# Optimization experiments

Measured on AMD Instinct MI355X. Metric: run time of the kernel, lower is better.

Reference implementation:

```python
import jax, jax.numpy as jnp
import numpy as np
from functools import partial

BLUR_K = 5
SIGMA = 1.5
DOWN = 4
SCALE = 5.0
OFFSET = 0.2

_DN = ('NCHW', 'OIHW', 'NCHW')


def _gaussian_kernel(k, sigma):
    x = jnp.arange(k, dtype=jnp.float32) - (k - 1) / 2.0
    g = jnp.exp(-x ** 2 / (2.0 * sigma ** 2))
    g2 = jnp.outer(g, g)
    g2 = g2 / g2.sum()
    return g2.reshape(1, 1, k, k)


def setup_inputs() -> dict:
    key = jax.random.key(0)
    left_rgb = jax.random.uniform(key, (16, 3, 544, 960), dtype=jnp.float32)
    return {"left_rgb": left_rgb}


def reference(left_rgb):
    B, C, H, W = left_rgb.shape
    # rgb -> gray (1x1 conv with fixed weights)
    w = jnp.array([0.2989, 0.587, 0.114], dtype=left_rgb.dtype)
    gray = jnp.einsum('bchw,c->bhw', left_rgb, w)[:, None]  # [B,1,H,W]

    # gaussian blur with reflect padding (torch F.pad mode='reflect')
    pad = BLUR_K // 2
    gray_p = jnp.pad(gray, ((0, 0), (0, 0), (pad, pad), (pad, pad)), mode='reflect')
    gk = _gaussian_kernel(BLUR_K, SIGMA).astype(left_rgb.dtype)
    gray_smooth = jax.lax.conv_general_dilated(gray_p, gk, (1, 1), 'VALID',
                                               dimension_numbers=_DN)

    # sobel gradients (cross-correlation, zero padding=1, same as torch conv2d)
    sx = jnp.array([[-1., 0., 1.], [-2., 0., 2.], [-1., 0., 1.]],
                   dtype=left_rgb.dtype).reshape(1, 1, 3, 3)
    sy = jnp.array([[-1., -2., -1.], [0., 0., 0.], [1., 2., 1.]],
                   dtype=left_rgb.dtype).reshape(1, 1, 3, 3)
    gx = jax.lax.conv_general_dilated(gray_smooth, sx, (1, 1), [(1, 1), (1, 1)],
                                      dimension_numbers=_DN)
    gy = jax.lax.conv_general_dilated(gray_smooth, sy, (1, 1), [(1, 1), (1, 1)],
                                      dimension_numbers=_DN)
    mag = jnp.sqrt(gx ** 2 + gy ** 2 + 1e-6)  # [B,1,H,W]

    # avg_pool2d kernel=stride=DOWN (H, W divisible by DOWN)
    down = mag.reshape(B, 1, H // DOWN, DOWN, W // DOWN, DOWN).mean(axis=(3, 5))

    edge_mask = jax.nn.sigmoid(SCALE * (down - OFFSET)) ** 2.0
    return edge_mask
```

## Files before the change

### kernel.cpp

```cpp
#include <hip/hip_runtime.h>
#include <cmath>

constexpr int B = 16, C = 3, H = 544, W = 960;
constexpr int OH = 136, OW = 240;
constexpr size_t HW = (size_t)H * W;

constexpr int TOH = 8, TOW = 30, NTH = 17, NTW = 8, MH = 32, MW = 120;
constexpr int GR = 40;
constexpr int GS = 132;
constexpr int NT = 5;
constexpr int NBLK = B * NTH * NTW;
constexpr int CPX = NBLK / 8;

__global__ __launch_bounds__(256, 2)
void edge_fused(const float* __restrict__ in, float* __restrict__ out,
                float gn0, float gn1, float gn2)
{
    __shared__ float gray[GR * GS];

    const int tid = threadIdx.x;
    const int blk = (blockIdx.x & 7) * CPX + (blockIdx.x >> 3);
    const int tw = blk % NTW;
    const int th = (blk / NTW) % NTH;
    const int b  = blk / (NTW * NTH);
    const int mh0 = th * MH, mw0 = tw * MW;
    const float* inb = in + (size_t)b * C * HW;

    float4 Rv[NT], Gv[NT], Bv[NT];
    #pragma unroll
    for (int k = 0; k < NT; ++k) {
        const int idx = tid + 256 * k;
        const int r = idx >> 5;
        const int c = idx & 31;
        int g = mh0 - 4 + r;
        g = g < 0 ? -g : (g >= H ? 2 * H - 2 - g : g);
        int gcb = mw0 - 4 + 4 * c;
        gcb = gcb < 0 ? 0 : (gcb > W - 4 ? W - 4 : gcb);
        const float* p = inb + (size_t)g * W + gcb;
        Rv[k] = *reinterpret_cast<const float4*>(p);
        Gv[k] = *reinterpret_cast<const float4*>(p + HW);
        Bv[k] = *reinterpret_cast<const float4*>(p + 2 * HW);
    }
    #pragma unroll
    for (int k = 0; k < NT; ++k) {
        const int idx = tid + 256 * k;
        const int r = idx >> 5;
        const int c = idx & 31;
        float4 g;
        g.x = fmaf(0.2989f, Rv[k].x, fmaf(0.587f, Gv[k].x, 0.114f * Bv[k].x));
        g.y = fmaf(0.2989f, Rv[k].y, fmaf(0.587f, Gv[k].y, 0.114f * Bv[k].y));
        g.z = fmaf(0.2989f, Rv[k].z, fmaf(0.587f, Gv[k].z, 0.114f * Bv[k].z));
        g.w = fmaf(0.2989f, Rv[k].w, fmaf(0.587f, Gv[k].w, 0.114f * Bv[k].w));
        const bool edgeq = (tw == 0 && c == 0) || (tw == NTW - 1 && c == 31);
        if (!edgeq)
            *reinterpret_cast<float4*>(&gray[r * GS + 4 * c]) = g;

        if (tw == 0) {
            const float nx = __shfl_down(g.x, 1, 32);
            if (c == 1)
                *reinterpret_cast<float4*>(&gray[r * GS]) =
                    make_float4(nx, g.w, g.z, g.y);
        } else if (tw == NTW - 1) {
            const float pw = __shfl_up(g.w, 1, 32);
            if (c == 30)
                *reinterpret_cast<float4*>(&gray[r * GS + 4 * 31]) =
                    make_float4(g.z, g.y, g.x, pw);
        }
    }
    __syncthreads();

    __builtin_amdgcn_s_setprio(1);
    if (tid < TOH * TOW) {
        const int orow = tid / TOW;
        const int ocol = tid - orow * TOW;
        const int lc0 = 4 * ocol;
        const int rb = 4 * orow + 1;

        float sm6[6][6];
        #pragma unroll
        for (int i = 0; i < 6; ++i)
            #pragma unroll
            for (int j = 0; j < 6; ++j) sm6[i][j] = 0.f;

        const float gk[5] = {gn0, gn1, gn2, gn1, gn0};
        #pragma unroll
        for (int tr = 0; tr < 10; ++tr) {
            const float* p = &gray[(rb + tr) * GS + lc0];
            const float4 u = *reinterpret_cast<const float4*>(p);
            const float4 v = *reinterpret_cast<const float4*>(p + 4);
            const float4 w = *reinterpret_cast<const float4*>(p + 8);
            const float t12[12] = {u.x, u.y, u.z, u.w, v.x, v.y, v.z, v.w,
                                   w.x, w.y, w.z, w.w};
            float h6[6];
            #pragma unroll
            for (int j = 0; j < 6; ++j)
                h6[j] = fmaf(gn0, t12[1 + j] + t12[5 + j],
                        fmaf(gn1, t12[2 + j] + t12[4 + j], gn2 * t12[3 + j]));
            #pragma unroll
            for (int i = 0; i < 6; ++i) {
                const int m = tr - i;
                if (m >= 0 && m < 5) {
                    #pragma unroll
                    for (int j = 0; j < 6; ++j)
                        sm6[i][j] = fmaf(gk[m], h6[j], sm6[i][j]);
                }
            }
        }

        #pragma unroll
        for (int i = 0; i < 6; ++i) {
            const int hh = mh0 + 4 * orow - 1 + i;
            const float rm = (hh >= 0 && hh < H) ? 1.f : 0.f;
            #pragma unroll
            for (int j = 0; j < 6; ++j) {
                const int ww = mw0 + 4 * ocol - 1 + j;
                sm6[i][j] *= rm * ((ww >= 0 && ww < W) ? 1.f : 0.f);
            }
        }

        float acc[4] = {0.f, 0.f, 0.f, 0.f};
        #pragma unroll
        for (int i = 0; i < 4; ++i) {
            #pragma unroll
            for (int j = 0; j < 4; ++j) {
                const float a00 = sm6[i][j],     a01 = sm6[i][j + 1],     a02 = sm6[i][j + 2];
                const float a10 = sm6[i + 1][j],                          a12 = sm6[i + 1][j + 2];
                const float a20 = sm6[i + 2][j], a21 = sm6[i + 2][j + 1], a22 = sm6[i + 2][j + 2];
                const float gx = (a02 - a00) + 2.f * (a12 - a10) + (a22 - a20);
                const float gy = (a20 + 2.f * a21 + a22) - (a00 + 2.f * a01 + a02);
                acc[i] += sqrtf(gx * gx + gy * gy + 1e-6f);
            }
        }
        const float down = ((acc[0] + acc[1]) + (acc[2] + acc[3])) * (1.f / 16.f);
        const float x = 5.0f * (down - 0.2f);
        const float sg = 1.f / (1.f + __expf(-x));
        const size_t o = ((size_t)b * OH + (th * TOH + orow)) * OW + (tw * TOW + ocol);
        out[o] = sg * sg;
    }
    __builtin_amdgcn_s_setprio(0);
}

extern "C" void kernel_launch(void* const* d_in, const int* in_sizes, int n_in,
                              void* d_out, int out_size, void* d_ws, size_t ws_size,
                              hipStream_t stream) {
    const float* in = (const float*)d_in[0];
    float* out = (float*)d_out;

    const double g0 = std::exp(-4.0 / 4.5);
    const double g1 = std::exp(-1.0 / 4.5);
    const double g2 = 1.0;
    const double S = 2.0 * (g0 + g1) + g2;
    const float gn0 = (float)(g0 / S);
    const float gn1 = (float)(g1 / S);
    const float gn2 = (float)(g2 / S);

    hipLaunchKernelGGL(edge_fused, dim3(NBLK), dim3(256), 0, stream,
                       in, out, gn0, gn1, gn2);
}
```

Before: 31.75 us.

## Restructure into per-wavefront 32x32 tiles without block-level barrier

Each 64-lane wavefront now owns an independent 32x32 input tile (8x8 outputs) with its own LDS slab, so the block-wide __syncthreads is replaced by wave-local lgkmcnt waits. Every lane produces one output, where previously only 240 of 256 threads did. The cost is a larger halo-to-tile ratio (40x40 loaded per 32x32), which means more redundant global reads, plus a partial 16-lane load and narrow 40-float rows that may cause LDS bank conflicts. Reflect padding at the left and right edges is now fixed up in LDS after the store rather than through shuffles.

Result: faster. 29.31 us, median of 2 (-7.7%).

```diff
diff --git a/kernel.cpp b/kernel.cpp
--- a/kernel.cpp
+++ b/kernel.cpp
@@ -5,76 +5,109 @@
 constexpr int OH = 136, OW = 240;
 constexpr size_t HW = (size_t)H * W;
 
-constexpr int TOH = 8, TOW = 30, NTH = 17, NTW = 8, MH = 32, MW = 120;
-constexpr int GR = 40;
-constexpr int GS = 132;
-constexpr int NT = 5;
-constexpr int NBLK = B * NTH * NTW;
+constexpr int TRW = 17;
+constexpr int TCW = 30;
+constexpr int NTILES = B * TRW * TCW;
+constexpr int WPB = 4;
+constexpr int NBLK = NTILES / WPB;
 constexpr int CPX = NBLK / 8;
 
-__global__ __launch_bounds__(256, 2)
-void edge_fused(const float* __restrict__ in, float* __restrict__ out,
-                float gn0, float gn1, float gn2)
+constexpr int GRr = 40;
+constexpr int GQ = 10;
+constexpr int GS2 = 44;
+
+__global__ __launch_bounds__(256)
+void edge_wave(const float* __restrict__ in, float* __restrict__ out,
+               float gn0, float gn1, float gn2)
 {
-    __shared__ float gray[GR * GS];
+    __shared__ float gray[WPB * GRr * GS2];
 
-    const int tid = threadIdx.x;
-    const int blk = (blockIdx.x & 7) * CPX + (blockIdx.x >> 3);
-    const int tw = blk % NTW;
-    const int th = (blk / NTW) % NTH;
-    const int b  = blk / (NTW * NTH);
-    const int mh0 = th * MH, mw0 = tw * MW;
+    const int tid  = threadIdx.x;
+    const int lane = tid & 63;
+    const int wv   = tid >> 6;
+    const int blk  = ((int)blockIdx.x & 7) * CPX + ((int)blockIdx.x >> 3);
+    const int t    = blk * WPB + wv;
+    const int tc   = t % TCW;
+    const int tr   = (t / TCW) % TRW;
+    const int b    = t / (TCW * TRW);
+    const int mh0  = tr * 32, mw0 = tc * 32;
     const float* inb = in + (size_t)b * C * HW;
+    float* gw = &gray[wv * GRr * GS2];
 
-    float4 Rv[NT], Gv[NT], Bv[NT];
+    float4 Rv[7], Gv[7], Bv[7];
     #pragma unroll
-    for (int k = 0; k < NT; ++k) {
-        const int idx = tid + 256 * k;
-        const int r = idx >> 5;
-        const int c = idx & 31;
+    for (int k = 0; k < 6; ++k) {
+        const int q = lane + 64 * k;
+        const int r = q / GQ, cq = q - r * GQ;
         int g = mh0 - 4 + r;
         g = g < 0 ? -g : (g >= H ? 2 * H - 2 - g : g);
-        int gcb = mw0 - 4 + 4 * c;
+        int gcb = mw0 - 4 + 4 * cq;
         gcb = gcb < 0 ? 0 : (gcb > W - 4 ? W - 4 : gcb);
         const float* p = inb + (size_t)g * W + gcb;
         Rv[k] = *reinterpret_cast<const float4*>(p);
         Gv[k] = *reinterpret_cast<const float4*>(p + HW);
         Bv[k] = *reinterpret_cast<const float4*>(p + 2 * HW);
     }
+    if (lane < 16) {
+        const int q = lane + 384;
+        const int r = q / GQ, cq = q - r * GQ;
+        int g = mh0 - 4 + r;
+        g = g < 0 ? -g : (g >= H ? 2 * H - 2 - g : g);
+        int gcb = mw0 - 4 + 4 * cq;
+        gcb = gcb < 0 ? 0 : (gcb > W - 4 ? W - 4 : gcb);
+        const float* p = inb + (size_t)g * W + gcb;
+        Rv[6] = *reinterpret_cast<const float4*>(p);
+        Gv[6] = *reinterpret_cast<const float4*>(p + HW);
+        Bv[6] = *reinterpret_cast<const float4*>(p + 2 * HW);
+    }
+
     #pragma unroll
-    for (int k = 0; k < NT; ++k) {
-        const int idx = tid + 256 * k;
-        const int r = idx >> 5;
-        const int c = idx & 31;
+    for (int k = 0; k < 6; ++k) {
+        const int q = lane + 64 * k;
+        const int r = q / GQ, cq = q - r * GQ;
         float4 g;
         g.x = fmaf(0.2989f, Rv[k].x, fmaf(0.587f, Gv[k].x, 0.114f * Bv[k].x));
         g.y = fmaf(0.2989f, Rv[k].y, fmaf(0.587f, Gv[k].y, 0.114f * Bv[k].y));
         g.z = fmaf(0.2989f, Rv[k].z, fmaf(0.587f, Gv[k].z, 0.114f * Bv[k].z));
         g.w = fmaf(0.2989f, Rv[k].w, fmaf(0.587f, Gv[k].w, 0.114f * Bv[k].w));
-        const bool edgeq = (tw == 0 && c == 0) || (tw == NTW - 1 && c == 31);
-        if (!edgeq)
-            *reinterpret_cast<float4*>(&gray[r * GS + 4 * c]) = g;
+        *reinterpret_cast<float4*>(&gw[r * GS2 + 4 * cq]) = g;
+    }
+    if (lane < 16) {
+        const int q = lane + 384;
+        const int r = q / GQ, cq = q - r * GQ;
+        float4 g;
+        g.x = fmaf(0.2989f, Rv[6].x, fmaf(0.587f, Gv[6].x, 0.114f * Bv[6].x));
+        g.y = fmaf(0.2989f, Rv[6].y, fmaf(0.587f, Gv[6].y, 0.114f * Bv[6].y));
+        g.z = fmaf(0.2989f, Rv[6].z, fmaf(0.587f, Gv[6].z, 0.114f * Bv[6].z));
+        g.w = fmaf(0.2989f, Rv[6].w, fmaf(0.587f, Gv[6].w, 0.114f * Bv[6].w));
+        *reinterpret_cast<float4*>(&gw[r * GS2 + 4 * cq]) = g;
+    }
 
-        if (tw == 0) {
-            const float nx = __shfl_down(g.x, 1, 32);
-            if (c == 1)
-                *reinterpret_cast<float4*>(&gray[r * GS]) =
-                    make_float4(nx, g.w, g.z, g.y);
-        } else if (tw == NTW - 1) {
-            const float pw = __shfl_up(g.w, 1, 32);
-            if (c == 30)
-                *reinterpret_cast<float4*>(&gray[r * GS + 4 * 31]) =
-                    make_float4(g.z, g.y, g.x, pw);
+    asm volatile("s_waitcnt lgkmcnt(0)" ::: "memory");
+    __builtin_amdgcn_sched_barrier(0);
+
+    if (tc == 0) {
+        if (lane < GRr) {
+            float* g_ = &gw[lane * GS2];
+            const float4 v = make_float4(g_[8], g_[7], g_[6], g_[5]);
+            *reinterpret_cast<float4*>(g_) = v;
+        }
+    } else if (tc == TCW - 1) {
+        if (lane < GRr) {
+            float* g_ = &gw[lane * GS2];
+            const float4 v = make_float4(g_[34], g_[33], g_[32], g_[31]);
+            *reinterpret_cast<float4*>(&g_[36]) = v;
         }
     }
-    __syncthreads();
+    asm volatile("s_waitcnt lgkmcnt(0)" ::: "memory");
+    __builtin_amdgcn_sched_barrier(0);
 
     __builtin_amdgcn_s_setprio(1);
-    if (tid < TOH * TOW) {
-        const int orow = tid / TOW;
-        const int ocol = tid - orow * TOW;
-        const int lc0 = 4 * ocol;
-        const int rb = 4 * orow + 1;
+    {
+        const int or_ = lane >> 3;
+        const int oc  = lane & 7;
+        const int rb  = 4 * or_ + 1;
+        const int lc0 = 4 * oc;
 
         float sm6[6][6];
         #pragma unroll
@@ -84,8 +117,8 @@
 
         const float gk[5] = {gn0, gn1, gn2, gn1, gn0};
         #pragma unroll
-        for (int tr = 0; tr < 10; ++tr) {
-            const float* p = &gray[(rb + tr) * GS + lc0];
+        for (int t2 = 0; t2 < 10; ++t2) {
+            const float* p = &gw[(rb + t2) * GS2 + lc0];
             const float4 u = *reinterpret_cast<const float4*>(p);
             const float4 v = *reinterpret_cast<const float4*>(p + 4);
             const float4 w = *reinterpret_cast<const float4*>(p + 8);
@@ -98,7 +131,7 @@
                         fmaf(gn1, t12[2 + j] + t12[4 + j], gn2 * t12[3 + j]));
             #pragma unroll
             for (int i = 0; i < 6; ++i) {
-                const int m = tr - i;
+                const int m = t2 - i;
                 if (m >= 0 && m < 5) {
                     #pragma unroll
                     for (int j = 0; j < 6; ++j)
@@ -109,11 +142,11 @@
 
         #pragma unroll
         for (int i = 0; i < 6; ++i) {
-            const int hh = mh0 + 4 * orow - 1 + i;
+            const int hh = mh0 + 4 * or_ - 1 + i;
             const float rm = (hh >= 0 && hh < H) ? 1.f : 0.f;
             #pragma unroll
             for (int j = 0; j < 6; ++j) {
-                const int ww = mw0 + 4 * ocol - 1 + j;
+                const int ww = mw0 + 4 * oc - 1 + j;
                 sm6[i][j] *= rm * ((ww >= 0 && ww < W) ? 1.f : 0.f);
             }
         }
@@ -134,8 +167,7 @@
         const float down = ((acc[0] + acc[1]) + (acc[2] + acc[3])) * (1.f / 16.f);
         const float x = 5.0f * (down - 0.2f);
         const float sg = 1.f / (1.f + __expf(-x));
-        const size_t o = ((size_t)b * OH + (th * TOH + orow)) * OW + (tw * TOW + ocol);
-        out[o] = sg * sg;
+        out[((size_t)b * OH + 8 * tr + or_) * OW + 8 * tc + oc] = sg * sg;
     }
     __builtin_amdgcn_s_setprio(0);
 }
@@ -154,6 +186,6 @@
     const float gn1 = (float)(g1 / S);
     const float gn2 = (float)(g2 / S);
 
-    hipLaunchKernelGGL(edge_fused, dim3(NBLK), dim3(256), 0, stream,
+    hipLaunchKernelGGL(edge_wave, dim3(NBLK), dim3(256), 0, stream,
                        in, out, gn0, gn1, gn2);
 }
```
